# Optimization experiments

Hardware: AMD Instinct MI355X
Metric: run time of the kernel (lower is better)

## Reference

```python
import jax, jax.numpy as jnp
import numpy as np

D_MODEL = 1024
NHEAD = 16
D_FF = 4096
SEQ = 2048
BATCH = 2
EPS = 1e-5


def _layernorm(x, g, b):
    mu = jnp.mean(x, axis=-1, keepdims=True)
    var = jnp.var(x, axis=-1, keepdims=True)
    return (x - mu) * jax.lax.rsqrt(var + EPS) * g + b


def setup_inputs() -> dict:
    key = jax.random.key(0)
    ks = jax.random.split(key, 16)
    s = 0.02
    def lin(k, din, dout):
        return jax.random.normal(k, (din, dout), jnp.float32) * s
    return {
        "x": jax.random.normal(ks[0], (SEQ, BATCH, D_MODEL), jnp.float32),
        "Wq": lin(ks[1], D_MODEL, D_MODEL), "bq": jnp.zeros((D_MODEL,), jnp.float32),
        "Wk": lin(ks[2], D_MODEL, D_MODEL), "bk": jnp.zeros((D_MODEL,), jnp.float32),
        "Wv": lin(ks[3], D_MODEL, D_MODEL), "bv": jnp.zeros((D_MODEL,), jnp.float32),
        "Wo": lin(ks[4], D_MODEL, D_MODEL), "bo": jnp.zeros((D_MODEL,), jnp.float32),
        "W1": lin(ks[5], D_MODEL, D_FF), "b1": jnp.zeros((D_FF,), jnp.float32),
        "W2": lin(ks[6], D_FF, D_MODEL), "b2": jnp.zeros((D_MODEL,), jnp.float32),
        "g1": jnp.ones((D_MODEL,), jnp.float32), "be1": jnp.zeros((D_MODEL,), jnp.float32),
        "g2": jnp.ones((D_MODEL,), jnp.float32), "be2": jnp.zeros((D_MODEL,), jnp.float32),
    }


def reference(x, Wq, bq, Wk, bk, Wv, bv, Wo, bo, W1, b1, W2, b2, g1, be1, g2, be2):
    # batch_first=False: x is [S, B, D] -> [B, S, D]
    xb = jnp.transpose(x, (1, 0, 2))
    B, S, D = xb.shape
    H, Dh = NHEAD, D // NHEAD

    Q = (xb @ Wq + bq).reshape(B, S, H, Dh)
    K = (xb @ Wk + bk).reshape(B, S, H, Dh)
    V = (xb @ Wv + bv).reshape(B, S, H, Dh)

    scores = jnp.einsum('bqhd,bkhd->bhqk', Q, K) / jnp.sqrt(jnp.float32(Dh))
    attn = jax.nn.softmax(scores, axis=-1)
    ctx = jnp.einsum('bhqk,bkhd->bqhd', attn, V).reshape(B, S, D)

    x_att = ctx @ Wo + bo
    xb = xb + x_att
    xb = _layernorm(xb, g1, be1)  # post-norm (norm_first=False)

    h = jax.nn.gelu(xb @ W1 + b1, approximate=False)
    xb = xb + (h @ W2 + b2)
    xb = _layernorm(xb, g2, be2)

    return jnp.transpose(xb, (1, 0, 2))  # back to [S, B, D]
```

## Files before the change

### kernel.cpp

```cpp
#include <hip/hip_runtime.h>
#include <hip/hip_bf16.h>
#include <cstdint>
#include <cstddef>

#define S_LEN 2048
#define BATCHN 2
#define DMODEL 1024
#define NHEADS 16
#define DHEAD 64
#define DFF 4096
#define NTOK (S_LEN*BATCHN)

typedef __bf16 bf16x8 __attribute__((ext_vector_type(8)));
typedef __bf16 bf16x4 __attribute__((ext_vector_type(4)));
typedef float f32x4 __attribute__((ext_vector_type(4)));
typedef __hip_bfloat16 bf16s;

#define QSCALE 0.18033688011112042592f

__device__ static inline void gload_lds16(const void* g, void* l) {
  __builtin_amdgcn_global_load_lds((const __attribute__((address_space(1))) void*)g,
                                   (__attribute__((address_space(3))) void*)l,
                                   16, 0, 0);
}


__global__ __launch_bounds__(256) void transpose_convert(const float* __restrict__ in,
                                                         bf16s* __restrict__ out,
                                                         int K, int N) {
  __shared__ float tile[32][33];
  const int tx = threadIdx.x & 31;
  const int ty = threadIdx.x >> 5;
  const int bx = blockIdx.x * 32;
  const int by = blockIdx.y * 32;
#pragma unroll
  for (int i = 0; i < 32; i += 8)
    tile[ty + i][tx] = in[(size_t)(by + ty + i) * N + bx + tx];
  __syncthreads();
#pragma unroll
  for (int i = 0; i < 32; i += 8)
    out[(size_t)(bx + ty + i) * K + by + tx] = __float2bfloat16(tile[tx][ty + i]);
}

__global__ __launch_bounds__(256) void cvt_bf16_kernel(const float* __restrict__ in,
                                                       bf16s* __restrict__ out, int n4) {
  int i = blockIdx.x * 256 + threadIdx.x;
  if (i < n4) {
    float4 v = ((const float4*)in)[i];
    union { bf16s h[4]; uint2 u; } pk;
    pk.h[0] = __float2bfloat16(v.x); pk.h[1] = __float2bfloat16(v.y);
    pk.h[2] = __float2bfloat16(v.z); pk.h[3] = __float2bfloat16(v.w);
    ((uint2*)out)[i] = pk.u;
  }
}

__global__ __launch_bounds__(256) void bias_concat_kernel(const float* __restrict__ bq,
                                                          const float* __restrict__ bk,
                                                          const float* __restrict__ bv,
                                                          float* __restrict__ bqkv) {
  int i = blockIdx.x * 256 + threadIdx.x;
  if (i < 3 * DMODEL) {
    float v = (i < DMODEL) ? bq[i] : (i < 2 * DMODEL ? bk[i - DMODEL] : bv[i - 2 * DMODEL]);
    bqkv[i] = v;
  }
}

template<int EPI>
__global__ __launch_bounds__(256, 2)
void gemm_kernel(const bf16s* __restrict__ A, const bf16s* __restrict__ Bt,
                 int M, int N, int K,
                 const float* __restrict__ bias,
                 const float* __restrict__ residF,
                 const bf16s* __restrict__ residB,
                 float* __restrict__ outF, bf16s* __restrict__ outB,
                 bf16s* __restrict__ Qb, bf16s* __restrict__ Kb, bf16s* __restrict__ Vtb)
{
  __shared__ bf16s smem[2][2 * 128 * 64];
  const int tid = threadIdx.x;
  const int l = tid & 63;
  const int w = tid >> 6;
  const int m0 = blockIdx.y * 128;
  const int n0 = blockIdx.x * 128;
  const int lr = l & 15, lg = l >> 4;

  f32x4 acc[4][4] = {};

  auto stageAB = [&](int buf, int kt) {
#pragma unroll
    for (int it = 0; it < 4; ++it) {
      int c = it * 4 + w;
      int off = c * 1024 + l * 16;
      int row = off >> 7;
      int kb = (off & 127) ^ ((row & 7) << 4);
      const char* srcA = (const char*)A + ((size_t)(m0 + row) * K + kt) * 2 + kb;
      gload_lds16(srcA, (char*)&smem[buf][0] + c * 1024);
      const char* srcB = (const char*)Bt + ((size_t)(n0 + row) * K + kt) * 2 + kb;
      gload_lds16(srcB, (char*)&smem[buf][0] + 16384 + c * 1024);
    }
  };

  auto compute = [&](int buf) {
    const char* base = (const char*)&smem[buf][0];
    const int wm = (w >> 1) * 64, wn = (w & 1) * 64;
#pragma unroll
    for (int kk = 0; kk < 2; ++kk) {
      bf16x8 af[4], bfr[4];
#pragma unroll
      for (int mi = 0; mi < 4; ++mi) {
        int row = wm + mi * 16 + lr;
        int kb = (kk * 64 + lg * 16) ^ ((row & 7) << 4);
        af[mi] = *(const bf16x8*)(base + row * 128 + kb);
      }
#pragma unroll
      for (int ni = 0; ni < 4; ++ni) {
        int row = wn + ni * 16 + lr;
        int kb = (kk * 64 + lg * 16) ^ ((row & 7) << 4);
        bfr[ni] = *(const bf16x8*)(base + 16384 + row * 128 + kb);
      }
#pragma unroll
      for (int mi = 0; mi < 4; ++mi)
#pragma unroll
        for (int ni = 0; ni < 4; ++ni)
          acc[mi][ni] = __builtin_amdgcn_mfma_f32_16x16x32_bf16(af[mi], bfr[ni], acc[mi][ni], 0, 0, 0);
    }
  };

  const int nt = K / 64;
  stageAB(0, 0);
  __syncthreads();
  int cur = 0;
  for (int t = 0; t < nt - 1; ++t) {
    stageAB(cur ^ 1, (t + 1) * 64);
    compute(cur);
    __syncthreads();
    cur ^= 1;
  }
  compute(cur);

  const int wm = (w >> 1) * 64, wn = (w & 1) * 64;
#pragma unroll
  for (int mi = 0; mi < 4; ++mi) {
#pragma unroll
    for (int ni = 0; ni < 4; ++ni) {
#pragma unroll
      for (int r = 0; r < 4; ++r) {
        int row = m0 + wm + mi * 16 + lg * 4 + r;
        int col = n0 + wn + ni * 16 + lr;
        float v = acc[mi][ni][r] + bias[col];
        if (EPI == 0) {
          int which = col >> 10;
          int h = (col & 1023) >> 6;
          int d = col & 63;
          int b = row & 1;
          int s = row >> 1;
          if (which == 0)
            Qb[(((size_t)(b * NHEADS + h)) * S_LEN + s) * DHEAD + d] = __float2bfloat16(v * QSCALE);
          else if (which == 1)
            Kb[(((size_t)(b * NHEADS + h)) * S_LEN + s) * DHEAD + d] = __float2bfloat16(v);
          else
            Vtb[(((size_t)(b * NHEADS + h)) * DHEAD + d) * S_LEN + s] = __float2bfloat16(v);
        } else if (EPI == 1) {
          outF[(size_t)row * N + col] = v + residF[(size_t)row * N + col];
        } else if (EPI == 2) {
          float gv = 0.5f * v * (1.0f + erff(v * 0.70710678118654752f));
          outB[(size_t)row * N + col] = __float2bfloat16(gv);
        } else {
          outF[(size_t)row * N + col] = v + __bfloat162float(residB[(size_t)row * N + col]);
        }
      }
    }
  }
}

__global__ __launch_bounds__(256, 2)
void attn_kernel(const bf16s* __restrict__ Qb, const bf16s* __restrict__ Kb,
                 const bf16s* __restrict__ Vtb, bf16s* __restrict__ ctx)
{
  __shared__ __align__(1024) char lds[51200];
  const int tid = threadIdx.x;
  const int l = tid & 63, w = tid >> 6;
  const int lr = l & 15, lg = l >> 4;

  int lin = blockIdx.x;
  int wg = (lin & 7) * 64 + (lin >> 3);
  int qb = wg & 15;
  int hb = wg >> 4;
  int h = hb & 15, b = hb >> 4;

  const char* Qg = (const char*)(Qb + ((size_t)(b * NHEADS + h)) * S_LEN * DHEAD);
  const char* Kg = (const char*)(Kb + ((size_t)(b * NHEADS + h)) * S_LEN * DHEAD);
  const char* Vg = (const char*)(Vtb + ((size_t)(b * NHEADS + h)) * DHEAD * S_LEN);

  const int swz = (lr & 7) << 4;
  const int aK0 = lr * 128 + ((lg * 16) ^ swz);
  const int aK1 = lr * 128 + ((64 + lg * 16) ^ swz);
  const int klane = (l >> 3) * 128  + (((l & 7) * 16) ^ ((l & 56) << 1));
  const int vlane = (l >> 3) * 4096 + (((l & 7) * 16) ^ ((l & 56) << 1));
  const int l16 = l * 16;
  char* Pw = lds + 32768 + w * 4608;
  const int pwA = lr * 144 + lg * 8;
  const int prA = lr * 144 + lg * 16;

  const int q0 = qb * 128 + w * 32;
  bf16x8 aq[2][2];
#pragma unroll
  for (int qi = 0; qi < 2; ++qi)
#pragma unroll
    for (int kk = 0; kk < 2; ++kk)
      aq[qi][kk] = *(const bf16x8*)(Qg + (size_t)(q0 + qi * 16 + lr) * 128 + kk * 64 + lg * 16);

  f32x4 o0[4] = {}, o1[4] = {};
  float m0 = -1e30f, m1 = -1e30f;
  float ls0 = 0.f, ls1 = 0.f;

  const int NT = S_LEN / 64;

  auto stage = [&](char* dK, int tile) {
    const char* kbg = Kg + (size_t)tile * 8192;
    const char* vbg = Vg + (size_t)tile * 128;
    char* dV = dK + 8192;
#pragma unroll
    for (int i = 0; i < 2; ++i) {
      int c = w * 2 + i;
      gload_lds16(kbg + c * 1024 + klane, dK + c * 1024 + l16);
      gload_lds16(vbg + (size_t)c * 32768 + vlane, dV + c * 1024 + l16);
    }
  };

  stage(lds, 0);
  asm volatile("s_waitcnt vmcnt(0)" ::: "memory");
  __builtin_amdgcn_s_barrier();

#define ATTN_ITER(BUF, t)                                                        \
  {                                                                              \
    int nxt = ((t) + 1 < NT) ? (t) + 1 : NT - 1;                                 \
    stage(lds + ((BUF) ^ 1) * 16384, nxt);                                       \
    const char* bK = lds + (BUF) * 16384;                                        \
    const char* bV = bK + 8192;                                                  \
    f32x4 st0[4], st1[4];                                                        \
    _Pragma("unroll")                                                            \
    for (int ni = 0; ni < 4; ++ni) {                                             \
      bf16x8 k0 = *(const bf16x8*)(bK + ni * 2048 + aK0);                        \
      bf16x8 k1 = *(const bf16x8*)(bK + ni * 2048 + aK1);                        \
      f32x4 z = {};                                                              \
      st0[ni] = __builtin_amdgcn_mfma_f32_16x16x32_bf16(k0, aq[0][0], z, 0, 0, 0);\
      st0[ni] = __builtin_amdgcn_mfma_f32_16x16x32_bf16(k1, aq[0][1], st0[ni], 0, 0, 0);\
      st1[ni] = __builtin_amdgcn_mfma_f32_16x16x32_bf16(k0, aq[1][0], z, 0, 0, 0);\
      st1[ni] = __builtin_amdgcn_mfma_f32_16x16x32_bf16(k1, aq[1][1], st1[ni], 0, 0, 0);\
    }                                                                            \
    f32x4 vm0 = st0[0], vm1 = st1[0];                                            \
    _Pragma("unroll")                                                            \
    for (int ni = 1; ni < 4; ++ni) {                                             \
      _Pragma("unroll")                                                          \
      for (int r = 0; r < 4; ++r) {                                              \
        vm0[r] = fmaxf(vm0[r], st0[ni][r]);                                      \
        vm1[r] = fmaxf(vm1[r], st1[ni][r]);                                      \
      }                                                                          \
    }                                                                            \
    float mx0 = fmaxf(fmaxf(vm0[0], vm0[1]), fmaxf(vm0[2], vm0[3]));             \
    float mx1 = fmaxf(fmaxf(vm1[0], vm1[1]), fmaxf(vm1[2], vm1[3]));             \
    mx0 = fmaxf(mx0, __shfl_xor(mx0, 16)); mx0 = fmaxf(mx0, __shfl_xor(mx0, 32));\
    mx1 = fmaxf(mx1, __shfl_xor(mx1, 16)); mx1 = fmaxf(mx1, __shfl_xor(mx1, 32));\
    if (!__all(mx0 <= m0 + 8.f && mx1 <= m1 + 8.f)) {                            \
      float nm0 = fmaxf(m0, mx0), nm1 = fmaxf(m1, mx1);                          \
      float al0 = exp2f(m0 - nm0), al1 = exp2f(m1 - nm1);                        \
      m0 = nm0; m1 = nm1; ls0 *= al0; ls1 *= al1;                                \
      _Pragma("unroll")                                                          \
      for (int r = 0; r < 4; ++r) {                                              \
        float s0r = __shfl(al0, lg * 4 + r);                                     \
        float s1r = __shfl(al1, lg * 4 + r);                                     \
        _Pragma("unroll")                                                        \
        for (int di = 0; di < 4; ++di) { o0[di][r] *= s0r; o1[di][r] *= s1r; }   \
      }                                                                          \
    }                                                                            \
    f32x4 ac0 = {}, ac1 = {};                                                    \
    _Pragma("unroll")                                                            \
    for (int ni = 0; ni < 4; ++ni) {                                             \
      _Pragma("unroll")                                                          \
      for (int r = 0; r < 4; ++r) {                                              \
        st0[ni][r] = exp2f(st0[ni][r] - m0);                                     \
        st1[ni][r] = exp2f(st1[ni][r] - m1);                                     \
      }                                                                          \
      ac0 += st0[ni]; ac1 += st1[ni];                                            \
    }                                                                            \
    ls0 += ac0[0] + ac0[1] + ac0[2] + ac0[3];                                    \
    ls1 += ac1[0] + ac1[1] + ac1[2] + ac1[3];                                    \
    _Pragma("unroll")                                                            \
    for (int ni = 0; ni < 4; ++ni) {                                             \
      bf16x4 p0, p1;                                                             \
      _Pragma("unroll")                                                          \
      for (int j = 0; j < 4; ++j) { p0[j] = (__bf16)st0[ni][j]; p1[j] = (__bf16)st1[ni][j]; }\
      *(bf16x4*)(Pw + pwA + ni * 32) = p0;                                       \
      *(bf16x4*)(Pw + 2304 + pwA + ni * 32) = p1;                                \
    }                                                                            \
    _Pragma("unroll")                                                            \
    for (int kk = 0; kk < 2; ++kk) {                                             \
      bf16x8 ap0 = *(const bf16x8*)(Pw + prA + kk * 64);                         \
      bf16x8 ap1 = *(const bf16x8*)(Pw + 2304 + prA + kk * 64);                  \
      const int av = kk ? aK1 : aK0;                                             \
      _Pragma("unroll")                                                          \
      for (int di = 0; di < 4; ++di) {                                           \
        bf16x8 vv = *(const bf16x8*)(bV + di * 2048 + av);                       \
        o0[di] = __builtin_amdgcn_mfma_f32_16x16x32_bf16(ap0, vv, o0[di], 0, 0, 0);\
        o1[di] = __builtin_amdgcn_mfma_f32_16x16x32_bf16(ap1, vv, o1[di], 0, 0, 0);\
      }                                                                          \
    }                                                                            \
    asm volatile("s_waitcnt vmcnt(0)" ::: "memory");                             \
    __builtin_amdgcn_s_barrier();                                                \
  }

  for (int t = 0; t < NT; t += 2) {
    ATTN_ITER(0, t);
    ATTN_ITER(1, t + 1);
  }
#undef ATTN_ITER

#pragma unroll
  for (int qi = 0; qi < 2; ++qi) {
    float ls = qi ? ls1 : ls0;
    ls += __shfl_xor(ls, 16);
    ls += __shfl_xor(ls, 32);
    float inv = 1.0f / ls;
#pragma unroll
    for (int r = 0; r < 4; ++r) {
      float invr = __shfl(inv, lg * 4 + r);
      int srow = q0 + qi * 16 + lg * 4 + r;
      int tkn = srow * BATCHN + b;
#pragma unroll
      for (int di = 0; di < 4; ++di) {
        int d = h * DHEAD + di * 16 + lr;
        float v = (qi ? o1[di][r] : o0[di][r]) * invr;
        ctx[(size_t)tkn * DMODEL + d] = __float2bfloat16(v);
      }
    }
  }
}

template<int OUTBF>
__global__ __launch_bounds__(256)
void ln_kernel(const float* __restrict__ in, const float* __restrict__ g,
               const float* __restrict__ be, float* __restrict__ outF,
               bf16s* __restrict__ outB)
{
  const int row = blockIdx.x;
  const int tid = threadIdx.x;
  const float* x = in + (size_t)row * DMODEL;
  float4 v = ((const float4*)x)[tid];
  float s = v.x + v.y + v.z + v.w;
  float s2 = v.x * v.x + v.y * v.y + v.z * v.z + v.w * v.w;
#pragma unroll
  for (int m = 1; m < 64; m <<= 1) { s += __shfl_xor(s, m); s2 += __shfl_xor(s2, m); }
  __shared__ float sm[8];
  const int wv = tid >> 6, l = tid & 63;
  if (l == 0) { sm[wv] = s; sm[4 + wv] = s2; }
  __syncthreads();
  s = sm[0] + sm[1] + sm[2] + sm[3];
  s2 = sm[4] + sm[5] + sm[6] + sm[7];
  float mean = s * (1.0f / DMODEL);
  float var = s2 * (1.0f / DMODEL) - mean * mean;
  float rstd = rsqrtf(var + 1e-5f);
  float4 gv = ((const float4*)g)[tid];
  float4 bv = ((const float4*)be)[tid];
  float o0 = (v.x - mean) * rstd * gv.x + bv.x;
  float o1 = (v.y - mean) * rstd * gv.y + bv.y;
  float o2 = (v.z - mean) * rstd * gv.z + bv.z;
  float o3 = (v.w - mean) * rstd * gv.w + bv.w;
  if (OUTBF) {
    union { bf16s h[4]; uint2 u; } pk;
    pk.h[0] = __float2bfloat16(o0); pk.h[1] = __float2bfloat16(o1);
    pk.h[2] = __float2bfloat16(o2); pk.h[3] = __float2bfloat16(o3);
    ((uint2*)(outB + (size_t)row * DMODEL))[tid] = pk.u;
  } else {
    float4 ov = {o0, o1, o2, o3};
    ((float4*)(outF + (size_t)row * DMODEL))[tid] = ov;
  }
}

extern "C" void kernel_launch(void* const* d_in, const int* in_sizes, int n_in,
                              void* d_out, int out_size, void* d_ws, size_t ws_size,
                              hipStream_t stream) {
  const float* x  = (const float*)d_in[0];
  const float* Wq = (const float*)d_in[1];
  const float* bq = (const float*)d_in[2];
  const float* Wk = (const float*)d_in[3];
  const float* bk = (const float*)d_in[4];
  const float* Wv = (const float*)d_in[5];
  const float* bv = (const float*)d_in[6];
  const float* Wo = (const float*)d_in[7];
  const float* bo = (const float*)d_in[8];
  const float* W1 = (const float*)d_in[9];
  const float* b1 = (const float*)d_in[10];
  const float* W2 = (const float*)d_in[11];
  const float* b2 = (const float*)d_in[12];
  const float* g1 = (const float*)d_in[13];
  const float* be1 = (const float*)d_in[14];
  const float* g2 = (const float*)d_in[15];
  const float* be2 = (const float*)d_in[16];

  char* ws = (char*)d_ws;
  size_t off = 0;
  auto alloc = [&](size_t bytes) -> void* {
    void* p = ws + off;
    off += (bytes + 255) & ~(size_t)255;
    return p;
  };
  bf16s* Wqkv_t = (bf16s*)alloc((size_t)3 * DMODEL * DMODEL * 2);
  bf16s* Wo_t   = (bf16s*)alloc((size_t)DMODEL * DMODEL * 2);
  bf16s* W1_t   = (bf16s*)alloc((size_t)DFF * DMODEL * 2);
  bf16s* W2_t   = (bf16s*)alloc((size_t)DMODEL * DFF * 2);
  float* bqkv   = (float*)alloc((size_t)3 * DMODEL * 4);
  bf16s* Xb     = (bf16s*)alloc((size_t)NTOK * DMODEL * 2);
  bf16s* Qb     = (bf16s*)alloc((size_t)NTOK * DMODEL * 2);
  bf16s* Kb     = (bf16s*)alloc((size_t)NTOK * DMODEL * 2);
  bf16s* Vtb    = (bf16s*)alloc((size_t)NTOK * DMODEL * 2);
  bf16s* ctx    = (bf16s*)alloc((size_t)NTOK * DMODEL * 2);
  float* s1     = (float*)alloc((size_t)NTOK * DMODEL * 4);
  bf16s* y1     = (bf16s*)alloc((size_t)NTOK * DMODEL * 2);
  bf16s* Hb     = (bf16s*)alloc((size_t)NTOK * DFF * 2);
  if (off > ws_size) return;

  transpose_convert<<<dim3(DMODEL / 32, DMODEL / 32), 256, 0, stream>>>(Wq, Wqkv_t, DMODEL, DMODEL);
  transpose_convert<<<dim3(DMODEL / 32, DMODEL / 32), 256, 0, stream>>>(Wk, Wqkv_t + (size_t)DMODEL * DMODEL, DMODEL, DMODEL);
  transpose_convert<<<dim3(DMODEL / 32, DMODEL / 32), 256, 0, stream>>>(Wv, Wqkv_t + (size_t)2 * DMODEL * DMODEL, DMODEL, DMODEL);
  transpose_convert<<<dim3(DMODEL / 32, DMODEL / 32), 256, 0, stream>>>(Wo, Wo_t, DMODEL, DMODEL);
  transpose_convert<<<dim3(DFF / 32, DMODEL / 32), 256, 0, stream>>>(W1, W1_t, DMODEL, DFF);
  transpose_convert<<<dim3(DMODEL / 32, DFF / 32), 256, 0, stream>>>(W2, W2_t, DFF, DMODEL);
  bias_concat_kernel<<<12, 256, 0, stream>>>(bq, bk, bv, bqkv);
  cvt_bf16_kernel<<<(NTOK * DMODEL / 4 + 255) / 256, 256, 0, stream>>>(x, Xb, NTOK * DMODEL / 4);

  gemm_kernel<0><<<dim3(3 * DMODEL / 128, NTOK / 128), 256, 0, stream>>>(
      Xb, Wqkv_t, NTOK, 3 * DMODEL, DMODEL, bqkv, nullptr, nullptr, nullptr, nullptr, Qb, Kb, Vtb);

  attn_kernel<<<512, 256, 0, stream>>>(Qb, Kb, Vtb, ctx);

  gemm_kernel<1><<<dim3(DMODEL / 128, NTOK / 128), 256, 0, stream>>>(
      ctx, Wo_t, NTOK, DMODEL, DMODEL, bo, x, nullptr, s1, nullptr, nullptr, nullptr, nullptr);
  ln_kernel<1><<<NTOK, 256, 0, stream>>>(s1, g1, be1, nullptr, y1);
  gemm_kernel<2><<<dim3(DFF / 128, NTOK / 128), 256, 0, stream>>>(
      y1, W1_t, NTOK, DFF, DMODEL, b1, nullptr, nullptr, nullptr, Hb, nullptr, nullptr, nullptr);
  gemm_kernel<3><<<dim3(DMODEL / 128, NTOK / 128), 256, 0, stream>>>(
      Hb, W2_t, NTOK, DMODEL, DFF, b2, nullptr, y1, s1, nullptr, nullptr, nullptr, nullptr);
  ln_kernel<0><<<NTOK, 256, 0, stream>>>(s1, g2, be2, (float*)d_out, nullptr);
}
```

Baseline: 396.8 us.

## Shrink GEMM K-tile and attention query tile to raise occupancy; fuse weight transposes

The GEMM K-tile drops from 64 to 32, halving LDS per block, and launch bounds target 3 blocks per CU. The attention kernel now processes 16 query rows per wave instead of 32, doubling the grid to 1024 blocks and shrinking the P buffer. The four square weight transposes are merged into one launch. More resident waves should hide latency better, but the GEMM now syncs twice as often per K step and attention reloads K/V tiles from LDS for half as many queries.

```diff
diff --git a/kernel.cpp b/kernel.cpp
--- a/kernel.cpp
+++ b/kernel.cpp
@@ -24,6 +24,27 @@
                                    16, 0, 0);
 }
 
+
+__global__ __launch_bounds__(256) void transpose_convert4(const float* __restrict__ s0,
+                                                          const float* __restrict__ s1,
+                                                          const float* __restrict__ s2,
+                                                          const float* __restrict__ s3,
+                                                          bf16s* __restrict__ dst) {
+  __shared__ float tile[32][33];
+  const float* in = (blockIdx.z == 0) ? s0 : (blockIdx.z == 1) ? s1 : (blockIdx.z == 2) ? s2 : s3;
+  bf16s* out = dst + (size_t)blockIdx.z * DMODEL * DMODEL;
+  const int tx = threadIdx.x & 31;
+  const int ty = threadIdx.x >> 5;
+  const int bx = blockIdx.x * 32;
+  const int by = blockIdx.y * 32;
+#pragma unroll
+  for (int i = 0; i < 32; i += 8)
+    tile[ty + i][tx] = in[(size_t)(by + ty + i) * DMODEL + bx + tx];
+  __syncthreads();
+#pragma unroll
+  for (int i = 0; i < 32; i += 8)
+    out[(size_t)(bx + ty + i) * DMODEL + by + tx] = __float2bfloat16(tile[tx][ty + i]);
+}
 
 __global__ __launch_bounds__(256) void transpose_convert(const float* __restrict__ in,
                                                          bf16s* __restrict__ out,
@@ -66,7 +87,7 @@
 }
 
 template<int EPI>
-__global__ __launch_bounds__(256, 2)
+__global__ __launch_bounds__(256, 3)
 void gemm_kernel(const bf16s* __restrict__ A, const bf16s* __restrict__ Bt,
                  int M, int N, int K,
                  const float* __restrict__ bias,
@@ -75,7 +96,7 @@
                  float* __restrict__ outF, bf16s* __restrict__ outB,
                  bf16s* __restrict__ Qb, bf16s* __restrict__ Kb, bf16s* __restrict__ Vtb)
 {
-  __shared__ bf16s smem[2][2 * 128 * 64];
+  __shared__ bf16s smem[2][8192];
   const int tid = threadIdx.x;
   const int l = tid & 63;
   const int w = tid >> 6;
@@ -86,58 +107,52 @@
   f32x4 acc[4][4] = {};
 
   auto stageAB = [&](int buf, int kt) {
-#pragma unroll
-    for (int it = 0; it < 4; ++it) {
-      int c = it * 4 + w;
+    char* base = (char*)&smem[buf][0];
+#pragma unroll
+    for (int i = 0; i < 2; ++i) {
+      int c = w * 2 + i;
       int off = c * 1024 + l * 16;
-      int row = off >> 7;
-      int kb = (off & 127) ^ ((row & 7) << 4);
-      const char* srcA = (const char*)A + ((size_t)(m0 + row) * K + kt) * 2 + kb;
-      gload_lds16(srcA, (char*)&smem[buf][0] + c * 1024);
-      const char* srcB = (const char*)Bt + ((size_t)(n0 + row) * K + kt) * 2 + kb;
-      gload_lds16(srcB, (char*)&smem[buf][0] + 16384 + c * 1024);
+      int row = off >> 6;
+      int kb = (off & 63) ^ ((row & 3) << 4);
+      gload_lds16((const char*)A + ((size_t)(m0 + row) * K + kt) * 2 + kb, base + off);
+      gload_lds16((const char*)Bt + ((size_t)(n0 + row) * K + kt) * 2 + kb, base + 8192 + off);
     }
   };
+
+  const int wm = (w >> 1) * 64, wn = (w & 1) * 64;
 
   auto compute = [&](int buf) {
     const char* base = (const char*)&smem[buf][0];
-    const int wm = (w >> 1) * 64, wn = (w & 1) * 64;
-#pragma unroll
-    for (int kk = 0; kk < 2; ++kk) {
-      bf16x8 af[4], bfr[4];
-#pragma unroll
-      for (int mi = 0; mi < 4; ++mi) {
-        int row = wm + mi * 16 + lr;
-        int kb = (kk * 64 + lg * 16) ^ ((row & 7) << 4);
-        af[mi] = *(const bf16x8*)(base + row * 128 + kb);
-      }
-#pragma unroll
-      for (int ni = 0; ni < 4; ++ni) {
-        int row = wn + ni * 16 + lr;
-        int kb = (kk * 64 + lg * 16) ^ ((row & 7) << 4);
-        bfr[ni] = *(const bf16x8*)(base + 16384 + row * 128 + kb);
-      }
-#pragma unroll
-      for (int mi = 0; mi < 4; ++mi)
-#pragma unroll
-        for (int ni = 0; ni < 4; ++ni)
-          acc[mi][ni] = __builtin_amdgcn_mfma_f32_16x16x32_bf16(af[mi], bfr[ni], acc[mi][ni], 0, 0, 0);
-    }
+    bf16x8 af[4], bfr[4];
+#pragma unroll
+    for (int mi = 0; mi < 4; ++mi) {
+      int row = wm + mi * 16 + lr;
+      af[mi] = *(const bf16x8*)(base + row * 64 + ((lg * 16) ^ ((row & 3) << 4)));
+    }
+#pragma unroll
+    for (int ni = 0; ni < 4; ++ni) {
+      int row = wn + ni * 16 + lr;
+      bfr[ni] = *(const bf16x8*)(base + 8192 + row * 64 + ((lg * 16) ^ ((row & 3) << 4)));
+    }
+#pragma unroll
+    for (int mi = 0; mi < 4; ++mi)
+#pragma unroll
+      for (int ni = 0; ni < 4; ++ni)
+        acc[mi][ni] = __builtin_amdgcn_mfma_f32_16x16x32_bf16(af[mi], bfr[ni], acc[mi][ni], 0, 0, 0);
   };
 
-  const int nt = K / 64;
+  const int nt = K / 32;
   stageAB(0, 0);
   __syncthreads();
   int cur = 0;
   for (int t = 0; t < nt - 1; ++t) {
-    stageAB(cur ^ 1, (t + 1) * 64);
+    stageAB(cur ^ 1, (t + 1) * 32);
     compute(cur);
     __syncthreads();
     cur ^= 1;
   }
   compute(cur);
 
-  const int wm = (w >> 1) * 64, wn = (w & 1) * 64;
 #pragma unroll
   for (int mi = 0; mi < 4; ++mi) {
 #pragma unroll
@@ -172,19 +187,19 @@
   }
 }
 
-__global__ __launch_bounds__(256, 2)
+__global__ __launch_bounds__(256, 3)
 void attn_kernel(const bf16s* __restrict__ Qb, const bf16s* __restrict__ Kb,
                  const bf16s* __restrict__ Vtb, bf16s* __restrict__ ctx)
 {
-  __shared__ __align__(1024) char lds[51200];
+  __shared__ __align__(1024) char lds[41984];
   const int tid = threadIdx.x;
   const int l = tid & 63, w = tid >> 6;
   const int lr = l & 15, lg = l >> 4;
 
   int lin = blockIdx.x;
-  int wg = (lin & 7) * 64 + (lin >> 3);
-  int qb = wg & 15;
-  int hb = wg >> 4;
+  int wg = (lin & 7) * 128 + (lin >> 3);
+  int qb = wg & 31;
+  int hb = wg >> 5;
   int h = hb & 15, b = hb >> 4;
 
   const char* Qg = (const char*)(Qb + ((size_t)(b * NHEADS + h)) * S_LEN * DHEAD);
@@ -197,21 +212,19 @@
   const int klane = (l >> 3) * 128  + (((l & 7) * 16) ^ ((l & 56) << 1));
   const int vlane = (l >> 3) * 4096 + (((l & 7) * 16) ^ ((l & 56) << 1));
   const int l16 = l * 16;
-  char* Pw = lds + 32768 + w * 4608;
+  char* Pw = lds + 32768 + w * 2304;
   const int pwA = lr * 144 + lg * 8;
   const int prA = lr * 144 + lg * 16;
 
-  const int q0 = qb * 128 + w * 32;
-  bf16x8 aq[2][2];
-#pragma unroll
-  for (int qi = 0; qi < 2; ++qi)
-#pragma unroll
-    for (int kk = 0; kk < 2; ++kk)
-      aq[qi][kk] = *(const bf16x8*)(Qg + (size_t)(q0 + qi * 16 + lr) * 128 + kk * 64 + lg * 16);
-
-  f32x4 o0[4] = {}, o1[4] = {};
-  float m0 = -1e30f, m1 = -1e30f;
-  float ls0 = 0.f, ls1 = 0.f;
+  const int q0 = qb * 64 + w * 16;
+  bf16x8 aq[2];
+#pragma unroll
+  for (int kk = 0; kk < 2; ++kk)
+    aq[kk] = *(const bf16x8*)(Qg + (size_t)(q0 + lr) * 128 + kk * 64 + lg * 16);
+
+  f32x4 o0[4] = {};
+  float m0 = -1e30f;
+  float ls0 = 0.f;
 
   const int NT = S_LEN / 64;
 
@@ -237,72 +250,57 @@
     stage(lds + ((BUF) ^ 1) * 16384, nxt);                                       \
     const char* bK = lds + (BUF) * 16384;                                        \
     const char* bV = bK + 8192;                                                  \
-    f32x4 st0[4], st1[4];                                                        \
+    f32x4 st0[4];                                                                \
     _Pragma("unroll")                                                            \
     for (int ni = 0; ni < 4; ++ni) {                                             \
       bf16x8 k0 = *(const bf16x8*)(bK + ni * 2048 + aK0);                        \
       bf16x8 k1 = *(const bf16x8*)(bK + ni * 2048 + aK1);                        \
       f32x4 z = {};                                                              \
-      st0[ni] = __builtin_amdgcn_mfma_f32_16x16x32_bf16(k0, aq[0][0], z, 0, 0, 0);\
-      st0[ni] = __builtin_amdgcn_mfma_f32_16x16x32_bf16(k1, aq[0][1], st0[ni], 0, 0, 0);\
-      st1[ni] = __builtin_amdgcn_mfma_f32_16x16x32_bf16(k0, aq[1][0], z, 0, 0, 0);\
-      st1[ni] = __builtin_amdgcn_mfma_f32_16x16x32_bf16(k1, aq[1][1], st1[ni], 0, 0, 0);\
-    }                                                                            \
-    f32x4 vm0 = st0[0], vm1 = st1[0];                                            \
+      st0[ni] = __builtin_amdgcn_mfma_f32_16x16x32_bf16(k0, aq[0], z, 0, 0, 0);  \
+      st0[ni] = __builtin_amdgcn_mfma_f32_16x16x32_bf16(k1, aq[1], st0[ni], 0, 0, 0);\
+    }                                                                            \
+    f32x4 vm0 = st0[0];                                                          \
     _Pragma("unroll")                                                            \
     for (int ni = 1; ni < 4; ++ni) {                                             \
       _Pragma("unroll")                                                          \
-      for (int r = 0; r < 4; ++r) {                                              \
-        vm0[r] = fmaxf(vm0[r], st0[ni][r]);                                      \
-        vm1[r] = fmaxf(vm1[r], st1[ni][r]);                                      \
-      }                                                                          \
+      for (int r = 0; r < 4; ++r) vm0[r] = fmaxf(vm0[r], st0[ni][r]);            \
     }                                                                            \
     float mx0 = fmaxf(fmaxf(vm0[0], vm0[1]), fmaxf(vm0[2], vm0[3]));             \
-    float mx1 = fmaxf(fmaxf(vm1[0], vm1[1]), fmaxf(vm1[2], vm1[3]));             \
     mx0 = fmaxf(mx0, __shfl_xor(mx0, 16)); mx0 = fmaxf(mx0, __shfl_xor(mx0, 32));\
-    mx1 = fmaxf(mx1, __shfl_xor(mx1, 16)); mx1 = fmaxf(mx1, __shfl_xor(mx1, 32));\
-    if (!__all(mx0 <= m0 + 8.f && mx1 <= m1 + 8.f)) {                            \
-      float nm0 = fmaxf(m0, mx0), nm1 = fmaxf(m1, mx1);                          \
-      float al0 = exp2f(m0 - nm0), al1 = exp2f(m1 - nm1);                        \
-      m0 = nm0; m1 = nm1; ls0 *= al0; ls1 *= al1;                                \
+    if (!__all(mx0 <= m0 + 8.f)) {                                               \
+      float nm0 = fmaxf(m0, mx0);                                                \
+      float al0 = exp2f(m0 - nm0);                                               \
+      m0 = nm0; ls0 *= al0;                                                      \
       _Pragma("unroll")                                                          \
       for (int r = 0; r < 4; ++r) {                                              \
         float s0r = __shfl(al0, lg * 4 + r);                                     \
-        float s1r = __shfl(al1, lg * 4 + r);                                     \
         _Pragma("unroll")                                                        \
-        for (int di = 0; di < 4; ++di) { o0[di][r] *= s0r; o1[di][r] *= s1r; }   \
+        for (int di = 0; di < 4; ++di) o0[di][r] *= s0r;                         \
       }                                                                          \
     }                                                                            \
-    f32x4 ac0 = {}, ac1 = {};                                                    \
+    f32x4 ac0 = {};                                                              \
     _Pragma("unroll")                                                            \
     for (int ni = 0; ni < 4; ++ni) {                                             \
       _Pragma("unroll")                                                          \
-      for (int r = 0; r < 4; ++r) {                                              \
-        st0[ni][r] = exp2f(st0[ni][r] - m0);                                     \
-        st1[ni][r] = exp2f(st1[ni][r] - m1);                                     \
-      }                                                                          \
-      ac0 += st0[ni]; ac1 += st1[ni];                                            \
+      for (int r = 0; r < 4; ++r) st0[ni][r] = exp2f(st0[ni][r] - m0);           \
+      ac0 += st0[ni];                                                            \
     }                                                                            \
     ls0 += ac0[0] + ac0[1] + ac0[2] + ac0[3];                                    \
-    ls1 += ac1[0] + ac1[1] + ac1[2] + ac1[3];                                    \
     _Pragma("unroll")                                                            \
     for (int ni = 0; ni < 4; ++ni) {                                             \
-      bf16x4 p0, p1;                                                             \
+      bf16x4 p0;                                                                 \
       _Pragma("unroll")                                                          \
-      for (int j = 0; j < 4; ++j) { p0[j] = (__bf16)st0[ni][j]; p1[j] = (__bf16)st1[ni][j]; }\
+      for (int j = 0; j < 4; ++j) p0[j] = (__bf16)st0[ni][j];                    \
       *(bf16x4*)(Pw + pwA + ni * 32) = p0;                                       \
-      *(bf16x4*)(Pw + 2304 + pwA + ni * 32) = p1;                                \
     }                                                                            \
     _Pragma("unroll")                                                            \
     for (int kk = 0; kk < 2; ++kk) {                                             \
       bf16x8 ap0 = *(const bf16x8*)(Pw + prA + kk * 64);                         \
-      bf16x8 ap1 = *(const bf16x8*)(Pw + 2304 + prA + kk * 64);                  \
       const int av = kk ? aK1 : aK0;                                             \
       _Pragma("unroll")                                                          \
       for (int di = 0; di < 4; ++di) {                                           \
         bf16x8 vv = *(const bf16x8*)(bV + di * 2048 + av);                       \
         o0[di] = __builtin_amdgcn_mfma_f32_16x16x32_bf16(ap0, vv, o0[di], 0, 0, 0);\
-        o1[di] = __builtin_amdgcn_mfma_f32_16x16x32_bf16(ap1, vv, o1[di], 0, 0, 0);\
       }                                                                          \
     }                                                                            \
     asm volatile("s_waitcnt vmcnt(0)" ::: "memory");                             \
@@ -315,22 +313,20 @@
   }
 #undef ATTN_ITER
 
-#pragma unroll
-  for (int qi = 0; qi < 2; ++qi) {
-    float ls = qi ? ls1 : ls0;
+  {
+    float ls = ls0;
     ls += __shfl_xor(ls, 16);
     ls += __shfl_xor(ls, 32);
     float inv = 1.0f / ls;
 #pragma unroll
     for (int r = 0; r < 4; ++r) {
       float invr = __shfl(inv, lg * 4 + r);
-      int srow = q0 + qi * 16 + lg * 4 + r;
+      int srow = q0 + lg * 4 + r;
       int tkn = srow * BATCHN + b;
 #pragma unroll
       for (int di = 0; di < 4; ++di) {
         int d = h * DHEAD + di * 16 + lr;
-        float v = (qi ? o1[di][r] : o0[di][r]) * invr;
-        ctx[(size_t)tkn * DMODEL + d] = __float2bfloat16(v);
+        ctx[(size_t)tkn * DMODEL + d] = __float2bfloat16(o0[di][r] * invr);
       }
     }
   }
@@ -419,10 +415,7 @@
   bf16s* Hb     = (bf16s*)alloc((size_t)NTOK * DFF * 2);
   if (off > ws_size) return;
 
-  transpose_convert<<<dim3(DMODEL / 32, DMODEL / 32), 256, 0, stream>>>(Wq, Wqkv_t, DMODEL, DMODEL);
-  transpose_convert<<<dim3(DMODEL / 32, DMODEL / 32), 256, 0, stream>>>(Wk, Wqkv_t + (size_t)DMODEL * DMODEL, DMODEL, DMODEL);
-  transpose_convert<<<dim3(DMODEL / 32, DMODEL / 32), 256, 0, stream>>>(Wv, Wqkv_t + (size_t)2 * DMODEL * DMODEL, DMODEL, DMODEL);
-  transpose_convert<<<dim3(DMODEL / 32, DMODEL / 32), 256, 0, stream>>>(Wo, Wo_t, DMODEL, DMODEL);
+  transpose_convert4<<<dim3(32, 32, 4), 256, 0, stream>>>(Wq, Wk, Wv, Wo, Wqkv_t);
   transpose_convert<<<dim3(DFF / 32, DMODEL / 32), 256, 0, stream>>>(W1, W1_t, DMODEL, DFF);
   transpose_convert<<<dim3(DMODEL / 32, DFF / 32), 256, 0, stream>>>(W2, W2_t, DFF, DMODEL);
   bias_concat_kernel<<<12, 256, 0, stream>>>(bq, bk, bv, bqkv);
@@ -431,7 +424,7 @@
   gemm_kernel<0><<<dim3(3 * DMODEL / 128, NTOK / 128), 256, 0, stream>>>(
       Xb, Wqkv_t, NTOK, 3 * DMODEL, DMODEL, bqkv, nullptr, nullptr, nullptr, nullptr, Qb, Kb, Vtb);
 
-  attn_kernel<<<512, 256, 0, stream>>>(Qb, Kb, Vtb, ctx);
+  attn_kernel<<<1024, 256, 0, stream>>>(Qb, Kb, Vtb, ctx);
 
   gemm_kernel<1><<<dim3(DMODEL / 128, NTOK / 128), 256, 0, stream>>>(
       ctx, Wo_t, NTOK, DMODEL, DMODEL, bo, x, nullptr, s1, nullptr, nullptr, nullptr, nullptr);
```

Measured after the change: 410.7 us. 3.5% more time.
